# Kernel optimization log

Measured on AMD Instinct MI355X. Metric: run time of the kernel, lower is better.

Reference implementation:

```python
import jax, jax.numpy as jnp
import numpy as np

G, N, D, H, R, O = 16384, 32, 128, 256, 32, 64  # graphs, nodes/graph, input_dim, hidden_dim, rank_dim, output_dim


def _xavier_uniform(key, shape):
    fan_in, fan_out = shape[0], shape[1]
    a = jnp.sqrt(6.0 / (fan_in + fan_out))
    return jax.random.uniform(key, shape, minval=-a, maxval=a, dtype=jnp.float32)


def setup_inputs() -> dict:
    key = jax.random.key(0)
    k_h, k_W, k_V, k_Wl, k_bl = jax.random.split(key, 5)
    h = jax.random.normal(k_h, (G, N, D), dtype=jnp.float32)
    W = _xavier_uniform(k_W, (D, R))          # graph_cp_pooling.W
    V = _xavier_uniform(k_V, (H, R))          # graph_cp_pooling.V
    Wl = _xavier_uniform(k_Wl, (O, H))        # linears_prediction[0].weight
    bl = jnp.zeros((O,), dtype=jnp.float32)   # linears_prediction[0].bias
    return {"h": h, "W": W, "V": V, "Wl": Wl, "bl": bl}


def reference(h, W, V, Wl, bl):
    # graph_cp_pooling (init=True), vectorized over graphs:
    #   feat_g = h_g @ W          -> [G, N, R]
    #   pooled = prod over nodes  -> [G, R]
    #   readout = pooled @ V.T    -> [G, H]
    feat = jnp.einsum('gnd,dr->gnr', h, W)
    pooled = jnp.prod(feat, axis=1)
    readout = pooled @ V.T
    # linears_prediction[0]; dropout is identity in eval mode
    score = readout @ Wl.T + bl
    return score
```

## Files before the change

kernel.cpp:

```cpp
#include <hip/hip_runtime.h>
#include <math.h>

#define NG  16384
#define NN  32
#define DD  128
#define RR  32
#define OO  64
#define HHH 256

__global__ void precompute_M_kernel(const float* __restrict__ Wl,
                                    const float* __restrict__ V,
                                    float* __restrict__ M) {
    int t = blockIdx.x * blockDim.x + threadIdx.x;
    int o = t >> 5;
    int r = t & 31;
    float s = 0.f;
#pragma unroll 8
    for (int hh = 0; hh < HHH; ++hh)
        s = fmaf(Wl[o * HHH + hh], V[hh * RR + r], s);
    M[o * RR + r] = s;
}

__device__ __forceinline__ void fma4(float4& a, float s, const float4& w) {
    a.x = fmaf(s, w.x, a.x);
    a.y = fmaf(s, w.y, a.y);
    a.z = fmaf(s, w.z, a.z);
    a.w = fmaf(s, w.w, a.w);
}

__global__ __launch_bounds__(256, 3)
void gin_main_kernel(const float* __restrict__ hsrc,
                     const float* __restrict__ W,
                     const float* __restrict__ M,
                     const float* __restrict__ bl,
                     float* __restrict__ out) {
    __shared__ float sW[DD * RR];

    const int tid  = threadIdx.x;
    const int lane = tid & 63;
    const int wv   = tid >> 6;

    {
        const float4* Wv  = (const float4*)W;
        float4*       sWv = (float4*)sW;
#pragma unroll
        for (int k = 0; k < 4; ++k) sWv[tid + k * 256] = Wv[tid + k * 256];
    }
    __syncthreads();

    const int rg = lane & 7;
    const int ng = lane >> 3;
    const int r0 = rg * 4;
    const float* pWb = sW + r0;
    const float blv = bl[lane];

    const int wave_global = blockIdx.x * 4 + wv;
    const int g0 = wave_global * 2;

#pragma unroll 1
    for (int gi = 0; gi < 2; ++gi) {
        const int g = g0 + gi;
        const float* hg  = hsrc + (size_t)g * (NN * DD);
        const float* hp0 = hg + (ng +  0) * DD;
        const float* hp1 = hg + (ng +  8) * DD;
        const float* hp2 = hg + (ng + 16) * DD;
        const float* hp3 = hg + (ng + 24) * DD;

        float4 acc0 = make_float4(0.f, 0.f, 0.f, 0.f);
        float4 acc1 = acc0, acc2 = acc0, acc3 = acc0;

#pragma unroll 2
        for (int dq = 0; dq < 32; ++dq) {
            const int d = dq * 4;
            float4 h0 = *(const float4*)(hp0 + d);
            float4 h1 = *(const float4*)(hp1 + d);
            float4 h2 = *(const float4*)(hp2 + d);
            float4 h3 = *(const float4*)(hp3 + d);
            float4 w0 = *(const float4*)(pWb + (d + 0) * RR);
            float4 w1 = *(const float4*)(pWb + (d + 1) * RR);
            float4 w2 = *(const float4*)(pWb + (d + 2) * RR);
            float4 w3 = *(const float4*)(pWb + (d + 3) * RR);
            fma4(acc0, h0.x, w0); fma4(acc0, h0.y, w1); fma4(acc0, h0.z, w2); fma4(acc0, h0.w, w3);
            fma4(acc1, h1.x, w0); fma4(acc1, h1.y, w1); fma4(acc1, h1.z, w2); fma4(acc1, h1.w, w3);
            fma4(acc2, h2.x, w0); fma4(acc2, h2.y, w1); fma4(acc2, h2.z, w2); fma4(acc2, h2.w, w3);
            fma4(acc3, h3.x, w0); fma4(acc3, h3.y, w1); fma4(acc3, h3.z, w2); fma4(acc3, h3.w, w3);
        }

        float4 p;
        p.x = acc0.x * acc1.x * acc2.x * acc3.x;
        p.y = acc0.y * acc1.y * acc2.y * acc3.y;
        p.z = acc0.z * acc1.z * acc2.z * acc3.z;
        p.w = acc0.w * acc1.w * acc2.w * acc3.w;
#pragma unroll
        for (int m = 8; m <= 32; m <<= 1) {
            p.x *= __shfl_xor(p.x, m);
            p.y *= __shfl_xor(p.y, m);
            p.z *= __shfl_xor(p.z, m);
            p.w *= __shfl_xor(p.w, m);
        }

        const float4* Mv = (const float4*)(M + lane * RR);
        float s = blv;
#pragma unroll
        for (int rq = 0; rq < 8; ++rq) {
            float4 pq;
            pq.x = __shfl(p.x, rq);
            pq.y = __shfl(p.y, rq);
            pq.z = __shfl(p.z, rq);
            pq.w = __shfl(p.w, rq);
            float4 m4 = Mv[rq];
            s = fmaf(pq.x, m4.x, s);
            s = fmaf(pq.y, m4.y, s);
            s = fmaf(pq.z, m4.z, s);
            s = fmaf(pq.w, m4.w, s);
        }
        out[(size_t)g * OO + lane] = s;
    }
}

extern "C" void kernel_launch(void* const* d_in, const int* in_sizes, int n_in,
                              void* d_out, int out_size, void* d_ws, size_t ws_size,
                              hipStream_t stream) {
    const float* h  = (const float*)d_in[0];
    const float* W  = (const float*)d_in[1];
    const float* V  = (const float*)d_in[2];
    const float* Wl = (const float*)d_in[3];
    const float* bl = (const float*)d_in[4];
    float* out = (float*)d_out;
    float* M   = (float*)d_ws;

    precompute_M_kernel<<<8, 256, 0, stream>>>(Wl, V, M);
    gin_main_kernel<<<2048, 256, 0, stream>>>(h, W, M, bl, out);
}
```

Before: 408.5 us.

## Process two graphs per wave concurrently with staggered d-loop start

The per-wave loop over two graphs is fused so both graphs' accumulators are updated in one d-loop, and each shared-memory W load is reused across 8 node rows instead of 4. The d index now starts at a lane-group-dependent offset and wraps, which staggers shared-memory reads across lanes to cut bank conflicts and spreads global-load addresses. Launch bounds are raised to 4 blocks per SM. The extra accumulators and h registers (about twice the live float4s) under a tighter register budget may cause spills.

```diff
diff --git a/kernel.cpp b/kernel.cpp
--- a/kernel.cpp
+++ b/kernel.cpp
@@ -28,7 +28,7 @@
     a.w = fmaf(s, w.w, a.w);
 }
 
-__global__ __launch_bounds__(256, 3)
+__global__ __launch_bounds__(256, 4)
 void gin_main_kernel(const float* __restrict__ hsrc,
                      const float* __restrict__ W,
                      const float* __restrict__ M,
@@ -55,42 +55,64 @@
     const float blv = bl[lane];
 
     const int wave_global = blockIdx.x * 4 + wv;
-    const int g0 = wave_global * 2;
+    const int gA = wave_global * 2;
+    const int gB = gA + 1;
 
-#pragma unroll 1
-    for (int gi = 0; gi < 2; ++gi) {
-        const int g = g0 + gi;
-        const float* hg  = hsrc + (size_t)g * (NN * DD);
-        const float* hp0 = hg + (ng +  0) * DD;
-        const float* hp1 = hg + (ng +  8) * DD;
-        const float* hp2 = hg + (ng + 16) * DD;
-        const float* hp3 = hg + (ng + 24) * DD;
+    const float* haB = hsrc + (size_t)gA * (NN * DD);
+    const float* hbB = hsrc + (size_t)gB * (NN * DD);
+    const float* ha0 = haB + (ng +  0) * DD;
+    const float* ha1 = haB + (ng +  8) * DD;
+    const float* ha2 = haB + (ng + 16) * DD;
+    const float* ha3 = haB + (ng + 24) * DD;
+    const float* hb0 = hbB + (ng +  0) * DD;
+    const float* hb1 = hbB + (ng +  8) * DD;
+    const float* hb2 = hbB + (ng + 16) * DD;
+    const float* hb3 = hbB + (ng + 24) * DD;
 
-        float4 acc0 = make_float4(0.f, 0.f, 0.f, 0.f);
-        float4 acc1 = acc0, acc2 = acc0, acc3 = acc0;
+    float4 aA0 = make_float4(0.f, 0.f, 0.f, 0.f);
+    float4 aA1 = aA0, aA2 = aA0, aA3 = aA0;
+    float4 aB0 = aA0, aB1 = aA0, aB2 = aA0, aB3 = aA0;
 
+    int d = rg * 4;
 #pragma unroll 2
-        for (int dq = 0; dq < 32; ++dq) {
-            const int d = dq * 4;
-            float4 h0 = *(const float4*)(hp0 + d);
-            float4 h1 = *(const float4*)(hp1 + d);
-            float4 h2 = *(const float4*)(hp2 + d);
-            float4 h3 = *(const float4*)(hp3 + d);
-            float4 w0 = *(const float4*)(pWb + (d + 0) * RR);
-            float4 w1 = *(const float4*)(pWb + (d + 1) * RR);
-            float4 w2 = *(const float4*)(pWb + (d + 2) * RR);
-            float4 w3 = *(const float4*)(pWb + (d + 3) * RR);
-            fma4(acc0, h0.x, w0); fma4(acc0, h0.y, w1); fma4(acc0, h0.z, w2); fma4(acc0, h0.w, w3);
-            fma4(acc1, h1.x, w0); fma4(acc1, h1.y, w1); fma4(acc1, h1.z, w2); fma4(acc1, h1.w, w3);
-            fma4(acc2, h2.x, w0); fma4(acc2, h2.y, w1); fma4(acc2, h2.z, w2); fma4(acc2, h2.w, w3);
-            fma4(acc3, h3.x, w0); fma4(acc3, h3.y, w1); fma4(acc3, h3.z, w2); fma4(acc3, h3.w, w3);
+    for (int dq = 0; dq < 32; ++dq) {
+        float4 hA0 = *(const float4*)(ha0 + d);
+        float4 hA1 = *(const float4*)(ha1 + d);
+        float4 hA2 = *(const float4*)(ha2 + d);
+        float4 hA3 = *(const float4*)(ha3 + d);
+        float4 hB0 = *(const float4*)(hb0 + d);
+        float4 hB1 = *(const float4*)(hb1 + d);
+        float4 hB2 = *(const float4*)(hb2 + d);
+        float4 hB3 = *(const float4*)(hb3 + d);
+        float4 w0 = *(const float4*)(pWb + (d + 0) * RR);
+        float4 w1 = *(const float4*)(pWb + (d + 1) * RR);
+        float4 w2 = *(const float4*)(pWb + (d + 2) * RR);
+        float4 w3 = *(const float4*)(pWb + (d + 3) * RR);
+        fma4(aA0, hA0.x, w0); fma4(aA0, hA0.y, w1); fma4(aA0, hA0.z, w2); fma4(aA0, hA0.w, w3);
+        fma4(aA1, hA1.x, w0); fma4(aA1, hA1.y, w1); fma4(aA1, hA1.z, w2); fma4(aA1, hA1.w, w3);
+        fma4(aA2, hA2.x, w0); fma4(aA2, hA2.y, w1); fma4(aA2, hA2.z, w2); fma4(aA2, hA2.w, w3);
+        fma4(aA3, hA3.x, w0); fma4(aA3, hA3.y, w1); fma4(aA3, hA3.z, w2); fma4(aA3, hA3.w, w3);
+        fma4(aB0, hB0.x, w0); fma4(aB0, hB0.y, w1); fma4(aB0, hB0.z, w2); fma4(aB0, hB0.w, w3);
+        fma4(aB1, hB1.x, w0); fma4(aB1, hB1.y, w1); fma4(aB1, hB1.z, w2); fma4(aB1, hB1.w, w3);
+        fma4(aB2, hB2.x, w0); fma4(aB2, hB2.y, w1); fma4(aB2, hB2.z, w2); fma4(aB2, hB2.w, w3);
+        fma4(aB3, hB3.x, w0); fma4(aB3, hB3.y, w1); fma4(aB3, hB3.z, w2); fma4(aB3, hB3.w, w3);
+        d = (d + 4) & 127;
+    }
+
+#pragma unroll
+    for (int side = 0; side < 2; ++side) {
+        float4 p;
+        if (side == 0) {
+            p.x = aA0.x * aA1.x * aA2.x * aA3.x;
+            p.y = aA0.y * aA1.y * aA2.y * aA3.y;
+            p.z = aA0.z * aA1.z * aA2.z * aA3.z;
+            p.w = aA0.w * aA1.w * aA2.w * aA3.w;
+        } else {
+            p.x = aB0.x * aB1.x * aB2.x * aB3.x;
+            p.y = aB0.y * aB1.y * aB2.y * aB3.y;
+            p.z = aB0.z * aB1.z * aB2.z * aB3.z;
+            p.w = aB0.w * aB1.w * aB2.w * aB3.w;
         }
-
-        float4 p;
-        p.x = acc0.x * acc1.x * acc2.x * acc3.x;
-        p.y = acc0.y * acc1.y * acc2.y * acc3.y;
-        p.z = acc0.z * acc1.z * acc2.z * acc3.z;
-        p.w = acc0.w * acc1.w * acc2.w * acc3.w;
 #pragma unroll
         for (int m = 8; m <= 32; m <<= 1) {
             p.x *= __shfl_xor(p.x, m);
@@ -114,7 +136,7 @@
             s = fmaf(pq.z, m4.z, s);
             s = fmaf(pq.w, m4.w, s);
         }
-        out[(size_t)g * OO + lane] = s;
+        out[(size_t)(side == 0 ? gA : gB) * OO + lane] = s;
     }
 }
 
```

Measured after the change: 760.1 us. 1.86x slower.
